# Kernel optimization log

Hardware: AMD Instinct MI355X
Metric: run time of the kernel (lower is better)

Reference implementation:

```python
import jax, jax.numpy as jnp
import numpy as np

D_MODEL = 1024
N_HEADS = 16
D_HEAD = D_MODEL // N_HEADS
B = 2
Q_LEN = 1024
MEM_LEN = 1024
K_LEN = MEM_LEN + Q_LEN


def _split_heads(x, n_heads):
    b, t, d = x.shape
    return x.reshape(b, t, n_heads, d // n_heads).transpose(0, 2, 1, 3)


def _rel_shift(x):
    # x: [b, h, q, k] -> Transformer-XL relative shift
    b, h, q_len, k_len = x.shape
    x = jnp.pad(x, ((0, 0), (0, 0), (0, 0), (1, 0)))
    x = x.reshape(b, h, k_len + 1, q_len)
    x = x[:, :, 1:, :]
    return x.reshape(b, h, q_len, k_len)


def setup_inputs() -> dict:
    key = jax.random.key(0)
    ks = jax.random.split(key, 10)
    s = 1.0 / np.sqrt(D_MODEL)  # lecun_normal-ish scale for kernels
    return {
        "h": jax.random.normal(ks[0], (B, Q_LEN, D_MODEL), jnp.float32),
        "mem": jax.random.normal(ks[1], (B, MEM_LEN, D_MODEL), jnp.float32),
        "r": jax.random.normal(ks[2], (K_LEN, D_MODEL), jnp.float32),
        "Wq": jax.random.normal(ks[3], (D_MODEL, D_MODEL), jnp.float32) * s,
        "Wk": jax.random.normal(ks[4], (D_MODEL, D_MODEL), jnp.float32) * s,
        "Wv": jax.random.normal(ks[5], (D_MODEL, D_MODEL), jnp.float32) * s,
        "Wr": jax.random.normal(ks[6], (D_MODEL, D_MODEL), jnp.float32) * s,
        "Wo": jax.random.normal(ks[7], (D_MODEL, D_MODEL), jnp.float32) * s,
        "r_w_bias": jnp.zeros((N_HEADS, D_HEAD), jnp.float32),
        "r_r_bias": jnp.zeros((N_HEADS, D_HEAD), jnp.float32),
    }


def reference(h, mem, r, Wq, Wk, Wv, Wr, Wo, r_w_bias, r_r_bias):
    k_len = mem.shape[1] + h.shape[1]
    cat = jnp.concatenate([mem, h], axis=1)           # [b, k, d]
    q = _split_heads(h @ Wq, N_HEADS)                  # [b, h, q, dh]
    k = _split_heads(cat @ Wk, N_HEADS)                # [b, h, k, dh]
    v = _split_heads(cat @ Wv, N_HEADS)                # [b, h, k, dh]
    r_head = (r @ Wr).reshape(k_len, N_HEADS, D_HEAD).transpose(1, 0, 2)  # [h, k, dh]

    qw = q + r_w_bias[None, :, None, :]
    ac = jnp.einsum('bhqd,bhkd->bhqk', qw, k)          # content score
    qr = q + r_r_bias[None, :, None, :]
    bd = _rel_shift(jnp.einsum('bhqd,hkd->bhqk', qr, r_head))  # position score

    attn_score = (ac + bd) / jnp.sqrt(jnp.array(D_HEAD, jnp.float32))
    attn_prob = jax.nn.softmax(attn_score, axis=-1)
    attn_vec = jnp.einsum('bhqk,bhkd->bhqd', attn_prob, v)
    b, nh, t, dh = attn_vec.shape
    attn_vec = attn_vec.transpose(0, 2, 1, 3).reshape(b, t, nh * dh)
    return attn_vec @ Wo
```

## Files before the change

kernel.cpp:

```cpp
#include <hip/hip_runtime.h>

#define DM 1024
#define NH 16
#define DH 64
#define QL 1024
#define KL 2048

typedef short s16x8 __attribute__((ext_vector_type(8)));
typedef float f32x4 __attribute__((ext_vector_type(4)));
typedef unsigned int u32x4 __attribute__((ext_vector_type(4)));

__device__ __forceinline__ unsigned short f2bf(float f) {
  unsigned int u = __builtin_bit_cast(unsigned int, f);
  u += 0x7fffu + ((u >> 16) & 1u);
  return (unsigned short)(u >> 16);
}
__device__ __forceinline__ float bf2f(unsigned short b) {
  unsigned int u = ((unsigned int)b) << 16;
  return __builtin_bit_cast(float, u);
}
__device__ __forceinline__ f32x4 mfma16(s16x8 a, s16x8 b, f32x4 c) {
  return __builtin_amdgcn_mfma_f32_16x16x32_bf16(a, b, c, 0, 0, 0);
}
__device__ __forceinline__ void gl2lds16(const void* g, void* l) {
  __builtin_amdgcn_global_load_lds(
      (const __attribute__((address_space(1))) unsigned int*)g,
      (__attribute__((address_space(3))) unsigned int*)l, 16, 0, 0);
}


__global__ __launch_bounds__(256) void prep_all(
    const float* __restrict__ h, const float* __restrict__ mem, const float* __restrict__ r,
    const float* __restrict__ Wq, const float* __restrict__ Wk, const float* __restrict__ Wv,
    const float* __restrict__ Wr, const float* __restrict__ Wo,
    unsigned short* __restrict__ catb, unsigned short* __restrict__ rb,
    unsigned short* __restrict__ wqt, unsigned short* __restrict__ wkvt,
    unsigned short* __restrict__ wrt,
    unsigned short* __restrict__ wohi, unsigned short* __restrict__ wolo)
{
  __shared__ unsigned short tH[64][72];
  __shared__ unsigned short tL[64][72];
  if (blockIdx.x < 6144) {
    int idx = blockIdx.x * 256 + threadIdx.x;
    if (idx < 1048576) {
      int e = idx * 4;
      int row = e >> 10, col = e & 1023;
      int b = row >> 11, t = row & 2047;
      const float* s = (t < 1024) ? &mem[((size_t)(b * 1024 + t)) * 1024 + col]
                                  : &h[((size_t)(b * 1024 + t - 1024)) * 1024 + col];
      float4 v = *(const float4*)s;
      *(ushort4*)&catb[e] = make_ushort4(f2bf(v.x), f2bf(v.y), f2bf(v.z), f2bf(v.w));
    } else {
      int e = (idx - 1048576) * 4;
      float4 v = *(const float4*)&r[e];
      *(ushort4*)&rb[e] = make_ushort4(f2bf(v.x), f2bf(v.y), f2bf(v.z), f2bf(v.w));
    }
    return;
  }
  int q = blockIdx.x - 6144;
  int job = q >> 8;
  int tb = q & 255;
  int sr0 = (tb >> 4) * 64, sc0 = (tb & 15) * 64;
  const float* src = (job == 0) ? Wq : (job == 1) ? Wk : (job == 2) ? Wv : (job == 3) ? Wr : Wo;
  int tid = threadIdx.x;
  int rr = tid >> 4, c4 = (tid & 15) * 4;
#pragma unroll
  for (int i = 0; i < 4; ++i) {
    int row = rr + i * 16;
    float4 v = *(const float4*)&src[(size_t)(sr0 + row) * 1024 + sc0 + c4];
    float vv[4] = {v.x, v.y, v.z, v.w};
#pragma unroll
    for (int j = 0; j < 4; ++j) {
      unsigned short hi = f2bf(vv[j]);
      tH[c4 + j][row] = hi;
      if (job == 4) tL[c4 + j][row] = f2bf(vv[j] - bf2f(hi));
    }
  }
  __syncthreads();
  unsigned short* dst = (job == 0) ? wqt : (job == 1) ? wkvt
                      : (job == 2) ? (wkvt + (size_t)1024 * 1024)
                      : (job == 3) ? wrt : wohi;
#pragma unroll
  for (int i = 0; i < 4; ++i) {
    int row = rr + i * 16;
    size_t o = (size_t)(sc0 + row) * 1024 + sr0 + c4;
    *(ushort4*)&dst[o] = make_ushort4(tH[row][c4], tH[row][c4 + 1], tH[row][c4 + 2], tH[row][c4 + 3]);
    if (job == 4)
      *(ushort4*)&wolo[o] = make_ushort4(tL[row][c4], tL[row][c4 + 1], tL[row][c4 + 2], tL[row][c4 + 3]);
  }
}

__global__ __launch_bounds__(256) void gemm_all(
    const unsigned short* __restrict__ catb, const unsigned short* __restrict__ rb,
    const unsigned short* __restrict__ wqt, const unsigned short* __restrict__ wkvt,
    const unsigned short* __restrict__ wrt,
    const float* __restrict__ rwb, const float* __restrict__ rrb,
    unsigned short* __restrict__ qwP, unsigned short* __restrict__ qrP,
    unsigned short* __restrict__ kP, unsigned short* __restrict__ vP,
    unsigned short* __restrict__ rP)
{
  __shared__ __align__(16) unsigned short As[2][128 * 32];
  __shared__ __align__(16) unsigned short Bs[2][128 * 32];
  int blk = blockIdx.x, tid = threadIdx.x;
  int job, mb, nb;
  const unsigned short *A, *Bt;
  if (blk < 128)      { job = 0; A = catb; Bt = wqt;  mb = blk >> 3; nb = blk & 7; }
  else if (blk < 640) { job = 1; A = catb; Bt = wkvt; int q = blk - 128; mb = q >> 4; nb = q & 15; }
  else                { job = 2; A = rb;   Bt = wrt;  int q = blk - 640; mb = q >> 3; nb = q & 7; }

  const int w = tid >> 6;
  const int r0 = tid >> 2;
  const int c0u = (tid & 3) * 8;
  int ga_r0 = mb * 128 + r0, ga_r1 = mb * 128 + 64 + r0;
  if (job == 0) {
    ga_r0 = ((ga_r0 >> 10) << 11) + 1024 + (ga_r0 & 1023);
    ga_r1 = ((ga_r1 >> 10) << 11) + 1024 + (ga_r1 & 1023);
  }
  const unsigned short* gA0 = A + (size_t)ga_r0 * 1024 + c0u;
  const unsigned short* gA1 = A + (size_t)ga_r1 * 1024 + c0u;
  const unsigned short* gB0 = Bt + (size_t)(nb * 128 + r0) * 1024 + c0u;
  const unsigned short* gB1 = Bt + (size_t)(nb * 128 + 64 + r0) * 1024 + c0u;

  const int lane = tid & 63;
  const int lc = lane & 15, quad = lane >> 4;
  const int wm = (w & 1) * 64, wn = (w >> 1) * 64;

  auto stage = [&](int k0, int bi) {
    gl2lds16(gA0 + k0, (char*)As[bi] + w * 1024);
    gl2lds16(gA1 + k0, (char*)As[bi] + 4096 + w * 1024);
    gl2lds16(gB0 + k0, (char*)Bs[bi] + w * 1024);
    gl2lds16(gB1 + k0, (char*)Bs[bi] + 4096 + w * 1024);
  };

  f32x4 acc[4][4];
#pragma unroll
  for (int mt = 0; mt < 4; ++mt)
#pragma unroll
    for (int nt = 0; nt < 4; ++nt) { acc[mt][nt][0] = 0.f; acc[mt][nt][1] = 0.f; acc[mt][nt][2] = 0.f; acc[mt][nt][3] = 0.f; }

  stage(0, 0);
  __syncthreads();
  for (int k0 = 0; k0 < 1024; k0 += 32) {
    int cur = (k0 >> 5) & 1;
    if (k0 + 32 < 1024) stage(k0 + 32, cur ^ 1);
    s16x8 af[4], bfr[4];
#pragma unroll
    for (int mt = 0; mt < 4; ++mt) af[mt] = *(const s16x8*)&As[cur][(wm + mt * 16 + lc) * 32 + quad * 8];
#pragma unroll
    for (int nt = 0; nt < 4; ++nt) bfr[nt] = *(const s16x8*)&Bs[cur][(wn + nt * 16 + lc) * 32 + quad * 8];
#pragma unroll
    for (int mt = 0; mt < 4; ++mt)
#pragma unroll
      for (int nt = 0; nt < 4; ++nt) acc[mt][nt] = mfma16(af[mt], bfr[nt], acc[mt][nt]);
    __syncthreads();
  }

#pragma unroll
  for (int mt = 0; mt < 4; ++mt) {
    int t4 = mb * 128 + wm + mt * 16 + quad * 4;
#pragma unroll
    for (int nt = 0; nt < 4; ++nt) {
      int n = nb * 128 + wn + nt * 16 + lc;
      if (job == 0) {
        int hh = n >> 6, dh = n & 63;
        int f = dh >> 5, qd = (dh >> 3) & 3, j = dh & 7;
        float bw = rwb[n], br = rrb[n];
        int bb = t4 >> 10, trow = t4 & 1023;
        size_t tbb = ((((size_t)(bb * NH + hh) * 64 + (trow >> 4)) * 2 + f) * 512) + qd * 128 + j;
        int l0 = trow & 15;
#pragma unroll
        for (int rr = 0; rr < 4; ++rr) {
          qwP[tbb + (l0 + rr) * 8] = f2bf(acc[mt][nt][rr] + bw);
          qrP[tbb + (l0 + rr) * 8] = f2bf(acc[mt][nt][rr] + br);
        }
      } else if (job == 1) {
        int bb = t4 >> 11, t = t4 & 2047;
        if (n < 1024) {
          int hh = n >> 6, dh = n & 63;
          int f = dh >> 5, qd = (dh >> 3) & 3, j = dh & 7;
          size_t tbb = ((((size_t)(bb * NH + hh) * 128 + (t >> 4)) * 2 + f) * 512) + qd * 128 + j;
          int l0 = t & 15;
#pragma unroll
          for (int rr = 0; rr < 4; ++rr)
            kP[tbb + (l0 + rr) * 8] = f2bf(acc[mt][nt][rr]);
        } else {
          int n2 = n - 1024, hh = n2 >> 6, dh = n2 & 63;
          int bhv = bb * NH + hh;
          int kt = t >> 5;
          int ntv = dh >> 4;
          int lanev = (((t >> 2) & 3) << 4) + (dh & 15);
          int elemv = ((t >> 4) & 1) << 2;
          ushort4 pk = make_ushort4(f2bf(acc[mt][nt][0]), f2bf(acc[mt][nt][1]),
                                    f2bf(acc[mt][nt][2]), f2bf(acc[mt][nt][3]));
          *(ushort4*)&vP[(((size_t)bhv * 64 + kt) * 4 + ntv) * 512 + lanev * 8 + elemv] = pk;
        }
      } else {
        int hh = n >> 6, dh = n & 63;
        int f = dh >> 5, qd = (dh >> 3) & 3, j = dh & 7;
        size_t tbb = (((size_t)hh * 128 + (t4 >> 4)) * 2 + f) * 512 + qd * 128 + j;
        int l0 = t4 & 15;
#pragma unroll
        for (int rr = 0; rr < 4; ++rr)
          rP[tbb + (l0 + rr) * 8] = f2bf(acc[mt][nt][rr]);
      }
    }
  }
}

#define BDSTR 2060
#define OSTR 65
__global__ __launch_bounds__(512, 4) void attn(
    const unsigned short* __restrict__ qwP, const unsigned short* __restrict__ qrP,
    const unsigned short* __restrict__ kP, const unsigned short* __restrict__ vP,
    const unsigned short* __restrict__ rP,
    unsigned short* __restrict__ avhi, unsigned short* __restrict__ avlo)
{
  __shared__ __align__(16) unsigned short bdS[16 * BDSTR];
  float* oS = (float*)bdS;
  float* lS = (float*)bdS + 8 * 16 * OSTR;

  const int tid = threadIdx.x;
  const int w = tid >> 6, lane = tid & 63;
  const int lc = lane & 15, quad = lane >> 4;
  const int sem = (blockIdx.x & 7) * 256 + (blockIdx.x >> 3);
  const int is = sem & 63, h = (sem >> 6) & 15, b = sem >> 10;
  const int i0 = is * 16;
  const size_t bh = (size_t)b * NH + h;

  const unsigned short* qwP_p = qwP + bh * 65536;
  const unsigned short* qrP_p = qrP + bh * 65536;
  const unsigned short* kP_p  = kP + bh * 131072;
  const unsigned short* vP_p  = vP + bh * (size_t)KL * DH + lane * 8;
  const unsigned short* rP_p  = rP + (size_t)h * 131072;

  if (tid < 16) {
    int kz = i0 + tid + 1025;
    if (kz < 2048) bdS[tid * BDSTR + kz] = 0;
  }

  {
    const int cmax = 1006 - i0;
    s16x8 qa00 = *(const s16x8*)(qrP_p + is * 1024 + lane * 8);
    s16x8 qa01 = *(const s16x8*)(qrP_p + is * 1024 + 512 + lane * 8);
    int r1 = i0 + 16 + lc; if (r1 > 1023) r1 = 1023;
    int off1 = (r1 >> 4) * 1024 + (quad * 16 + (r1 & 15)) * 8;
    s16x8 qa10 = *(const s16x8*)(qrP_p + off1);
    s16x8 qa11 = *(const s16x8*)(qrP_p + off1 + 512);
    const int xt0 = w * 16;
    const unsigned short* rp = rP_p + xt0 * 1024 + lane * 8;
    s16x8 rf0 = *(const s16x8*)rp;
    s16x8 rf1 = *(const s16x8*)(rp + 512);
    const int rbq = quad * 4 * BDSTR;
    for (int xt = xt0; xt < xt0 + 16; ++xt) {
      s16x8 cf0 = rf0, cf1 = rf1;
      if (xt + 1 < xt0 + 16) {
        const unsigned short* rpn = rP_p + (xt + 1) * 1024 + lane * 8;
        rf0 = *(const s16x8*)rpn;
        rf1 = *(const s16x8*)(rpn + 512);
      }
      f32x4 c0; c0[0] = 0.f; c0[1] = 0.f; c0[2] = 0.f; c0[3] = 0.f;
      c0 = mfma16(qa00, cf0, c0); c0 = mfma16(qa01, cf1, c0);
      int c = xt * 16 + lc;
#pragma unroll
      for (int rr = 0; rr < 4; ++rr) {
        int row = quad * 4 + rr;
        int s = c + i0 + row - 1023;
        int off = (s < 0) ? (s - 12) : s;
        if (!(row == 0 && s < 0))
          bdS[rbq + rr * BDSTR + off] = f2bf(c0[rr]);
      }
      if (xt * 16 <= cmax) {
        f32x4 c1; c1[0] = 0.f; c1[1] = 0.f; c1[2] = 0.f; c1[3] = 0.f;
        c1 = mfma16(qa10, cf0, c1); c1 = mfma16(qa11, cf1, c1);
        if (lane < 16) {
          int key2 = c + i0 + 1041;
          if (key2 < 2048) bdS[15 * BDSTR + key2] = f2bf(c1[0]);
        }
      }
    }
  }
  __syncthreads();

  s16x8 qwf0 = *(const s16x8*)(qwP_p + is * 1024 + lane * 8);
  s16x8 qwf1 = *(const s16x8*)(qwP_p + is * 1024 + 512 + lane * 8);

  f32x4 O[4];
#pragma unroll
  for (int nt = 0; nt < 4; ++nt) { O[nt][0] = 0.f; O[nt][1] = 0.f; O[nt][2] = 0.f; O[nt][3] = 0.f; }
  float lsumQ = 0.f;

  const unsigned short* bdlane = bdS + lc * BDSTR + quad * 4;
  const int base = w * 256;
  const float E2S = 0.18033688011112042f;
  const float E2B = -17.312340490667562f;

  auto loadK4 = [&](int k0, s16x8& a0, s16x8& a1, s16x8& b0, s16x8& b1) {
    const unsigned short* kp = kP_p + (size_t)(k0 >> 4) * 1024 + lane * 8;
    a0 = *(const s16x8*)kp;
    a1 = *(const s16x8*)(kp + 512);
    b0 = *(const s16x8*)(kp + 1024);
    b1 = *(const s16x8*)(kp + 1536);
  };
  auto loadV4 = [&](int k0, s16x8& x0, s16x8& x1, s16x8& x2, s16x8& x3) {
    const unsigned short* bp = vP_p + (size_t)(k0 >> 5) * 2048;
    x0 = *(const s16x8*)bp;
    x1 = *(const s16x8*)(bp + 512);
    x2 = *(const s16x8*)(bp + 1024);
    x3 = *(const s16x8*)(bp + 1536);
  };

  s16x8 ka0, ka1, kb0, kb1, v0, v1, v2, v3;
  uint2 bq0 = *(const uint2*)(bdlane + base);
  uint2 bq1 = *(const uint2*)(bdlane + base + 16);
  loadK4(base, ka0, ka1, kb0, kb1);
  loadV4(base, v0, v1, v2, v3);

#pragma unroll 1
  for (int s = 0; s < 8; ++s) {
    const int k0 = base + s * 32;
    const int kn = (s < 7) ? (k0 + 32) : k0;
    uint2 nq0 = *(const uint2*)(bdlane + kn);
    uint2 nq1 = *(const uint2*)(bdlane + kn + 16);
    s16x8 na0, na1, nb0, nb1;  loadK4(kn, na0, na1, nb0, nb1);
    s16x8 nv0, nv1, nv2, nv3;  loadV4(kn, nv0, nv1, nv2, nv3);

    __builtin_amdgcn_s_setprio(1);
    f32x4 c;
    c[0] = __builtin_bit_cast(float, bq0.x << 16);
    c[1] = __builtin_bit_cast(float, bq0.x & 0xFFFF0000u);
    c[2] = __builtin_bit_cast(float, bq0.y << 16);
    c[3] = __builtin_bit_cast(float, bq0.y & 0xFFFF0000u);
    c = mfma16(ka0, qwf0, c);
    c = mfma16(ka1, qwf1, c);
    f32x4 d;
    d[0] = __builtin_bit_cast(float, bq1.x << 16);
    d[1] = __builtin_bit_cast(float, bq1.x & 0xFFFF0000u);
    d[2] = __builtin_bit_cast(float, bq1.y << 16);
    d[3] = __builtin_bit_cast(float, bq1.y & 0xFFFF0000u);
    d = mfma16(kb0, qwf0, d);
    d = mfma16(kb1, qwf1, d);
    __builtin_amdgcn_s_setprio(0);

    float p0[4], p1[4];
#pragma unroll
    for (int rr = 0; rr < 4; ++rr) {
      p0[rr] = __builtin_amdgcn_exp2f(fmaf(c[rr], E2S, E2B));
      p1[rr] = __builtin_amdgcn_exp2f(fmaf(d[rr], E2S, E2B));
    }
    lsumQ += ((p0[0] + p0[1]) + (p0[2] + p0[3])) + ((p1[0] + p1[1]) + (p1[2] + p1[3]));

    unsigned int w0, w1, w2, w3;
    asm("v_cvt_pk_bf16_f32 %0, %1, %2" : "=v"(w0) : "v"(p0[0]), "v"(p0[1]));
    asm("v_cvt_pk_bf16_f32 %0, %1, %2" : "=v"(w1) : "v"(p0[2]), "v"(p0[3]));
    asm("v_cvt_pk_bf16_f32 %0, %1, %2" : "=v"(w2) : "v"(p1[0]), "v"(p1[1]));
    asm("v_cvt_pk_bf16_f32 %0, %1, %2" : "=v"(w3) : "v"(p1[2]), "v"(p1[3]));
    u32x4 pw4 = {w0, w1, w2, w3};
    s16x8 pf = __builtin_bit_cast(s16x8, pw4);

    __builtin_amdgcn_s_setprio(1);
    O[0] = mfma16(v0, pf, O[0]);
    O[1] = mfma16(v1, pf, O[1]);
    O[2] = mfma16(v2, pf, O[2]);
    O[3] = mfma16(v3, pf, O[3]);
    __builtin_amdgcn_s_setprio(0);

    bq0 = nq0; bq1 = nq1;
    ka0 = na0; ka1 = na1; kb0 = nb0; kb1 = nb1;
    v0 = nv0; v1 = nv1; v2 = nv2; v3 = nv3;
  }

  lsumQ += __shfl_xor(lsumQ, 16);
  lsumQ += __shfl_xor(lsumQ, 32);

  __syncthreads();
#pragma unroll
  for (int nt = 0; nt < 4; ++nt)
#pragma unroll
    for (int rr = 0; rr < 4; ++rr)
      oS[(w * 16 + lc) * OSTR + nt * 16 + quad * 4 + rr] = O[nt][rr];
  if (lane < 16) lS[w * 16 + lc] = lsumQ;
  __syncthreads();

  if (tid < 256) {
    int r = tid >> 4, c0 = (tid & 15) * 4;
    float L = 0.f, a0 = 0.f, a1 = 0.f, a2 = 0.f, a3 = 0.f;
#pragma unroll
    for (int wv = 0; wv < 8; ++wv) {
      L += lS[wv * 16 + r];
      const float* op = oS + (wv * 16 + r) * OSTR + c0;
      a0 += op[0]; a1 += op[1]; a2 += op[2]; a3 += op[3];
    }
    float inv = 1.0f / L;
    float v[4] = {a0 * inv, a1 * inv, a2 * inv, a3 * inv};
    unsigned short hi[4], lo[4];
#pragma unroll
    for (int j = 0; j < 4; ++j) {
      hi[j] = f2bf(v[j]);
      lo[j] = f2bf(v[j] - bf2f(hi[j]));
    }
    size_t oidx = ((size_t)(b * QL + i0 + r)) * DM + h * DH + c0;
    *(ushort4*)&avhi[oidx] = make_ushort4(hi[0], hi[1], hi[2], hi[3]);
    *(ushort4*)&avlo[oidx] = make_ushort4(lo[0], lo[1], lo[2], lo[3]);
  }
}

__global__ __launch_bounds__(256) void gemm_final(
    const unsigned short* __restrict__ avhi, const unsigned short* __restrict__ avlo,
    const unsigned short* __restrict__ wohi, const unsigned short* __restrict__ wolo,
    float* __restrict__ out)
{
  __shared__ __align__(16) unsigned short S[2][4][64 * 32];
  int tid = threadIdx.x;
  int sem = (blockIdx.x & 7) * 64 + (blockIdx.x >> 3);
  int mb = sem >> 4, nb = sem & 15;

  const int w = tid >> 6, lane = tid & 63;
  const int srow = w * 16 + (lane >> 2);
  const int scu = (lane & 3) * 8;
  const size_t arow = (size_t)(mb * 64 + srow) * 1024 + scu;
  const size_t brow = (size_t)(nb * 64 + srow) * 1024 + scu;

  const int lc = lane & 15, quad = lane >> 4;
  const int wm = (w & 1) * 32, wn = (w >> 1) * 32;

  auto stage = [&](int k0, int bi) {
    gl2lds16(avhi + arow + k0, (char*)S[bi][0] + w * 1024);
    gl2lds16(avlo + arow + k0, (char*)S[bi][1] + w * 1024);
    gl2lds16(wohi + brow + k0, (char*)S[bi][2] + w * 1024);
    gl2lds16(wolo + brow + k0, (char*)S[bi][3] + w * 1024);
  };

  f32x4 acc[2][2];
#pragma unroll
  for (int mt = 0; mt < 2; ++mt)
#pragma unroll
    for (int nt = 0; nt < 2; ++nt) { acc[mt][nt][0] = 0.f; acc[mt][nt][1] = 0.f; acc[mt][nt][2] = 0.f; acc[mt][nt][3] = 0.f; }

  stage(0, 0);
  __syncthreads();
  for (int k0 = 0; k0 < 1024; k0 += 32) {
    int cur = (k0 >> 5) & 1;
    if (k0 + 32 < 1024) stage(k0 + 32, cur ^ 1);
    s16x8 ah[2], al[2], bh[2], bl[2];
#pragma unroll
    for (int mt = 0; mt < 2; ++mt) {
      int off = (wm + mt * 16 + lc) * 32 + quad * 8;
      ah[mt] = *(const s16x8*)&S[cur][0][off];
      al[mt] = *(const s16x8*)&S[cur][1][off];
    }
#pragma unroll
    for (int nt = 0; nt < 2; ++nt) {
      int off = (wn + nt * 16 + lc) * 32 + quad * 8;
      bh[nt] = *(const s16x8*)&S[cur][2][off];
      bl[nt] = *(const s16x8*)&S[cur][3][off];
    }
#pragma unroll
    for (int mt = 0; mt < 2; ++mt)
#pragma unroll
      for (int nt = 0; nt < 2; ++nt) {
        acc[mt][nt] = mfma16(ah[mt], bh[nt], acc[mt][nt]);
        acc[mt][nt] = mfma16(ah[mt], bl[nt], acc[mt][nt]);
        acc[mt][nt] = mfma16(al[mt], bh[nt], acc[mt][nt]);
      }
    __syncthreads();
  }

#pragma unroll
  for (int mt = 0; mt < 2; ++mt)
#pragma unroll
    for (int nt = 0; nt < 2; ++nt) {
      int n = nb * 64 + wn + nt * 16 + lc;
#pragma unroll
      for (int rr = 0; rr < 4; ++rr) {
        int m = mb * 64 + wm + mt * 16 + quad * 4 + rr;
        out[(size_t)m * 1024 + n] = acc[mt][nt][rr];
      }
    }
}

extern "C" void kernel_launch(void* const* d_in, const int* in_sizes, int n_in,
                              void* d_out, int out_size, void* d_ws, size_t ws_size,
                              hipStream_t stream) {
  (void)in_sizes; (void)n_in; (void)out_size; (void)ws_size;
  const float* h   = (const float*)d_in[0];
  const float* mem = (const float*)d_in[1];
  const float* r   = (const float*)d_in[2];
  const float* Wq  = (const float*)d_in[3];
  const float* Wk  = (const float*)d_in[4];
  const float* Wv  = (const float*)d_in[5];
  const float* Wr  = (const float*)d_in[6];
  const float* Wo  = (const float*)d_in[7];
  const float* rwb = (const float*)d_in[8];
  const float* rrb = (const float*)d_in[9];
  float* out = (float*)d_out;

  char* ws = (char*)d_ws;
  unsigned short* catb = (unsigned short*)(ws + 0);
  unsigned short* rb   = (unsigned short*)(ws + 8388608);
  unsigned short* wqt  = (unsigned short*)(ws + 12582912);
  unsigned short* wkvt = (unsigned short*)(ws + 14680064);
  unsigned short* wrt  = (unsigned short*)(ws + 18874368);
  unsigned short* wohi = (unsigned short*)(ws + 20971520);
  unsigned short* wolo = (unsigned short*)(ws + 23068672);
  unsigned short* qwP  = (unsigned short*)(ws + 25165824);
  unsigned short* qrP  = (unsigned short*)(ws + 29360128);
  unsigned short* kPb  = (unsigned short*)(ws + 33554432);
  unsigned short* vPb  = (unsigned short*)(ws + 41943040);
  unsigned short* rPb  = (unsigned short*)(ws + 50331648);
  unsigned short* avhi = (unsigned short*)(ws + 54525952);
  unsigned short* avlo = (unsigned short*)(ws + 58720256);

  prep_all<<<7424, 256, 0, stream>>>(h, mem, r, Wq, Wk, Wv, Wr, Wo,
                                     catb, rb, wqt, wkvt, wrt, wohi, wolo);
  gemm_all<<<768, 256, 0, stream>>>(catb, rb, wqt, wkvt, wrt, rwb, rrb,
                                    qwP, qrP, kPb, vPb, rPb);
  attn<<<2048, 512, 0, stream>>>(qwP, qrP, kPb, vPb, rPb, avhi, avlo);
  gemm_final<<<512, 256, 0, stream>>>(avhi, avlo, wohi, wolo, out);
}
```

Before: 229.2 us.

## Split bd score buffer into two key halves to halve LDS and raise occupancy

The attention kernel now builds the relative-position score buffer in shared memory for one half of the key range at a time. It computes that half's positional scores and then runs the QK/softmax/PV loop over it. This halves the LDS footprint (row stride 2060 to 1060), so launch bounds go from 4 to 6 blocks per CU for more occupancy. The cost is an extra barrier pair per half, more complex index mapping for the shifted positions, and rP fetches that are no longer software-prefetched. The setprio hints around the MFMAs were also removed.

```diff
diff --git a/kernel.cpp b/kernel.cpp
--- a/kernel.cpp
+++ b/kernel.cpp
@@ -207,9 +207,9 @@
   }
 }
 
-#define BDSTR 2060
+#define BDSTR 1060
 #define OSTR 65
-__global__ __launch_bounds__(512, 4) void attn(
+__global__ __launch_bounds__(512, 6) void attn(
     const unsigned short* __restrict__ qwP, const unsigned short* __restrict__ qrP,
     const unsigned short* __restrict__ kP, const unsigned short* __restrict__ vP,
     const unsigned short* __restrict__ rP,
@@ -233,54 +233,6 @@
   const unsigned short* vP_p  = vP + bh * (size_t)KL * DH + lane * 8;
   const unsigned short* rP_p  = rP + (size_t)h * 131072;
 
-  if (tid < 16) {
-    int kz = i0 + tid + 1025;
-    if (kz < 2048) bdS[tid * BDSTR + kz] = 0;
-  }
-
-  {
-    const int cmax = 1006 - i0;
-    s16x8 qa00 = *(const s16x8*)(qrP_p + is * 1024 + lane * 8);
-    s16x8 qa01 = *(const s16x8*)(qrP_p + is * 1024 + 512 + lane * 8);
-    int r1 = i0 + 16 + lc; if (r1 > 1023) r1 = 1023;
-    int off1 = (r1 >> 4) * 1024 + (quad * 16 + (r1 & 15)) * 8;
-    s16x8 qa10 = *(const s16x8*)(qrP_p + off1);
-    s16x8 qa11 = *(const s16x8*)(qrP_p + off1 + 512);
-    const int xt0 = w * 16;
-    const unsigned short* rp = rP_p + xt0 * 1024 + lane * 8;
-    s16x8 rf0 = *(const s16x8*)rp;
-    s16x8 rf1 = *(const s16x8*)(rp + 512);
-    const int rbq = quad * 4 * BDSTR;
-    for (int xt = xt0; xt < xt0 + 16; ++xt) {
-      s16x8 cf0 = rf0, cf1 = rf1;
-      if (xt + 1 < xt0 + 16) {
-        const unsigned short* rpn = rP_p + (xt + 1) * 1024 + lane * 8;
-        rf0 = *(const s16x8*)rpn;
-        rf1 = *(const s16x8*)(rpn + 512);
-      }
-      f32x4 c0; c0[0] = 0.f; c0[1] = 0.f; c0[2] = 0.f; c0[3] = 0.f;
-      c0 = mfma16(qa00, cf0, c0); c0 = mfma16(qa01, cf1, c0);
-      int c = xt * 16 + lc;
-#pragma unroll
-      for (int rr = 0; rr < 4; ++rr) {
-        int row = quad * 4 + rr;
-        int s = c + i0 + row - 1023;
-        int off = (s < 0) ? (s - 12) : s;
-        if (!(row == 0 && s < 0))
-          bdS[rbq + rr * BDSTR + off] = f2bf(c0[rr]);
-      }
-      if (xt * 16 <= cmax) {
-        f32x4 c1; c1[0] = 0.f; c1[1] = 0.f; c1[2] = 0.f; c1[3] = 0.f;
-        c1 = mfma16(qa10, cf0, c1); c1 = mfma16(qa11, cf1, c1);
-        if (lane < 16) {
-          int key2 = c + i0 + 1041;
-          if (key2 < 2048) bdS[15 * BDSTR + key2] = f2bf(c1[0]);
-        }
-      }
-    }
-  }
-  __syncthreads();
-
   s16x8 qwf0 = *(const s16x8*)(qwP_p + is * 1024 + lane * 8);
   s16x8 qwf1 = *(const s16x8*)(qwP_p + is * 1024 + 512 + lane * 8);
 
@@ -290,7 +242,8 @@
   float lsumQ = 0.f;
 
   const unsigned short* bdlane = bdS + lc * BDSTR + quad * 4;
-  const int base = w * 256;
+  const int rbq = quad * 4 * BDSTR;
+  const int cmax = 1006 - i0;
   const float E2S = 0.18033688011112042f;
   const float E2B = -17.312340490667562f;
 
@@ -309,64 +262,130 @@
     x3 = *(const s16x8*)(bp + 1536);
   };
 
-  s16x8 ka0, ka1, kb0, kb1, v0, v1, v2, v3;
-  uint2 bq0 = *(const uint2*)(bdlane + base);
-  uint2 bq1 = *(const uint2*)(bdlane + base + 16);
-  loadK4(base, ka0, ka1, kb0, kb1);
-  loadV4(base, v0, v1, v2, v3);
-
 #pragma unroll 1
-  for (int s = 0; s < 8; ++s) {
-    const int k0 = base + s * 32;
-    const int kn = (s < 7) ? (k0 + 32) : k0;
-    uint2 nq0 = *(const uint2*)(bdlane + kn);
-    uint2 nq1 = *(const uint2*)(bdlane + kn + 16);
-    s16x8 na0, na1, nb0, nb1;  loadK4(kn, na0, na1, nb0, nb1);
-    s16x8 nv0, nv1, nv2, nv3;  loadV4(kn, nv0, nv1, nv2, nv3);
-
-    __builtin_amdgcn_s_setprio(1);
-    f32x4 c;
-    c[0] = __builtin_bit_cast(float, bq0.x << 16);
-    c[1] = __builtin_bit_cast(float, bq0.x & 0xFFFF0000u);
-    c[2] = __builtin_bit_cast(float, bq0.y << 16);
-    c[3] = __builtin_bit_cast(float, bq0.y & 0xFFFF0000u);
-    c = mfma16(ka0, qwf0, c);
-    c = mfma16(ka1, qwf1, c);
-    f32x4 d;
-    d[0] = __builtin_bit_cast(float, bq1.x << 16);
-    d[1] = __builtin_bit_cast(float, bq1.x & 0xFFFF0000u);
-    d[2] = __builtin_bit_cast(float, bq1.y << 16);
-    d[3] = __builtin_bit_cast(float, bq1.y & 0xFFFF0000u);
-    d = mfma16(kb0, qwf0, d);
-    d = mfma16(kb1, qwf1, d);
-    __builtin_amdgcn_s_setprio(0);
-
-    float p0[4], p1[4];
-#pragma unroll
-    for (int rr = 0; rr < 4; ++rr) {
-      p0[rr] = __builtin_amdgcn_exp2f(fmaf(c[rr], E2S, E2B));
-      p1[rr] = __builtin_amdgcn_exp2f(fmaf(d[rr], E2S, E2B));
-    }
-    lsumQ += ((p0[0] + p0[1]) + (p0[2] + p0[3])) + ((p1[0] + p1[1]) + (p1[2] + p1[3]));
-
-    unsigned int w0, w1, w2, w3;
-    asm("v_cvt_pk_bf16_f32 %0, %1, %2" : "=v"(w0) : "v"(p0[0]), "v"(p0[1]));
-    asm("v_cvt_pk_bf16_f32 %0, %1, %2" : "=v"(w1) : "v"(p0[2]), "v"(p0[3]));
-    asm("v_cvt_pk_bf16_f32 %0, %1, %2" : "=v"(w2) : "v"(p1[0]), "v"(p1[1]));
-    asm("v_cvt_pk_bf16_f32 %0, %1, %2" : "=v"(w3) : "v"(p1[2]), "v"(p1[3]));
-    u32x4 pw4 = {w0, w1, w2, w3};
-    s16x8 pf = __builtin_bit_cast(s16x8, pw4);
-
-    __builtin_amdgcn_s_setprio(1);
-    O[0] = mfma16(v0, pf, O[0]);
-    O[1] = mfma16(v1, pf, O[1]);
-    O[2] = mfma16(v2, pf, O[2]);
-    O[3] = mfma16(v3, pf, O[3]);
-    __builtin_amdgcn_s_setprio(0);
-
-    bq0 = nq0; bq1 = nq1;
-    ka0 = na0; ka1 = na1; kb0 = nb0; kb1 = nb1;
-    v0 = nv0; v1 = nv1; v2 = nv2; v3 = nv3;
+  for (int H = 0; H < 2; ++H) {
+    if (H) __syncthreads();
+
+    if (H && tid < 16) {
+      int kz = i0 + tid + 1025;
+      if (kz < 2048) bdS[tid * BDSTR + (kz - 1024)] = 0;
+    }
+    {
+      s16x8 qa00 = *(const s16x8*)(qrP_p + is * 1024 + lane * 8);
+      s16x8 qa01 = *(const s16x8*)(qrP_p + is * 1024 + 512 + lane * 8);
+      int n, xA_hi = 0, xB_lo = 0, xbase = 0;
+      if (H == 0) {
+        xbase = (1008 - i0) >> 4;
+        n = ((2046 - i0) >> 4) - xbase + 1;
+      } else {
+        xA_hi = (1022 - i0) >> 4;
+        xB_lo = (2032 - i0) >> 4;
+        n = (xA_hi + 1) + (128 - xB_lo);
+      }
+      s16x8 qa10, qa11;
+      if (H) {
+        int r1 = i0 + 16 + lc; if (r1 > 1023) r1 = 1023;
+        int off1 = (r1 >> 4) * 1024 + (quad * 16 + (r1 & 15)) * 8;
+        qa10 = *(const s16x8*)(qrP_p + off1);
+        qa11 = *(const s16x8*)(qrP_p + off1 + 512);
+      }
+#pragma unroll 1
+      for (int j = 0; j < 9; ++j) {
+        int t = w + 8 * j;
+        if (t >= n) break;
+        int xt = (H == 0) ? (xbase + t)
+                          : ((t <= xA_hi) ? t : (xB_lo + (t - xA_hi - 1)));
+        const unsigned short* rp = rP_p + xt * 1024 + lane * 8;
+        s16x8 cf0 = *(const s16x8*)rp;
+        s16x8 cf1 = *(const s16x8*)(rp + 512);
+        f32x4 c0; c0[0] = 0.f; c0[1] = 0.f; c0[2] = 0.f; c0[3] = 0.f;
+        c0 = mfma16(qa00, cf0, c0); c0 = mfma16(qa01, cf1, c0);
+        int c = xt * 16 + lc;
+        if (H == 0) {
+#pragma unroll
+          for (int rr = 0; rr < 4; ++rr) {
+            int row = quad * 4 + rr;
+            int s = c + i0 + row - 1023;
+            if ((unsigned)s < 1024u)
+              bdS[rbq + rr * BDSTR + s] = f2bf(c0[rr]);
+          }
+        } else {
+#pragma unroll
+          for (int rr = 0; rr < 4; ++rr) {
+            int s = c + i0 + quad * 4 + rr - 1023;
+            int off = (s >= 1024) ? (s - 1024) : (s - 36);
+            if (s >= 1024 || (s < 0 && (quad | rr) != 0))
+              bdS[rbq + rr * BDSTR + off] = f2bf(c0[rr]);
+          }
+          if (xt * 16 <= cmax) {
+            f32x4 c1; c1[0] = 0.f; c1[1] = 0.f; c1[2] = 0.f; c1[3] = 0.f;
+            c1 = mfma16(qa10, cf0, c1); c1 = mfma16(qa11, cf1, c1);
+            if (lane < 16) {
+              int key2 = c + i0 + 1041;
+              if (key2 < 2048) bdS[15 * BDSTR + (key2 - 1024)] = f2bf(c1[0]);
+            }
+          }
+        }
+      }
+    }
+    __syncthreads();
+
+    const int kg0 = H * 1024 + w * 128;
+    const int kc0 = w * 128;
+    s16x8 ka0, ka1, kb0, kb1, v0, v1, v2, v3;
+    uint2 bq0 = *(const uint2*)(bdlane + kc0);
+    uint2 bq1 = *(const uint2*)(bdlane + kc0 + 16);
+    loadK4(kg0, ka0, ka1, kb0, kb1);
+    loadV4(kg0, v0, v1, v2, v3);
+
+#pragma unroll 1
+    for (int s = 0; s < 4; ++s) {
+      const int dn = (s < 3) ? (s + 1) * 32 : s * 32;
+      uint2 nq0 = *(const uint2*)(bdlane + kc0 + dn);
+      uint2 nq1 = *(const uint2*)(bdlane + kc0 + dn + 16);
+      s16x8 na0, na1, nb0, nb1;  loadK4(kg0 + dn, na0, na1, nb0, nb1);
+      s16x8 nv0, nv1, nv2, nv3;  loadV4(kg0 + dn, nv0, nv1, nv2, nv3);
+
+      f32x4 c;
+      c[0] = __builtin_bit_cast(float, bq0.x << 16);
+      c[1] = __builtin_bit_cast(float, bq0.x & 0xFFFF0000u);
+      c[2] = __builtin_bit_cast(float, bq0.y << 16);
+      c[3] = __builtin_bit_cast(float, bq0.y & 0xFFFF0000u);
+      c = mfma16(ka0, qwf0, c);
+      c = mfma16(ka1, qwf1, c);
+      f32x4 d;
+      d[0] = __builtin_bit_cast(float, bq1.x << 16);
+      d[1] = __builtin_bit_cast(float, bq1.x & 0xFFFF0000u);
+      d[2] = __builtin_bit_cast(float, bq1.y << 16);
+      d[3] = __builtin_bit_cast(float, bq1.y & 0xFFFF0000u);
+      d = mfma16(kb0, qwf0, d);
+      d = mfma16(kb1, qwf1, d);
+
+      float p0[4], p1[4];
+#pragma unroll
+      for (int rr = 0; rr < 4; ++rr) {
+        p0[rr] = __builtin_amdgcn_exp2f(fmaf(c[rr], E2S, E2B));
+        p1[rr] = __builtin_amdgcn_exp2f(fmaf(d[rr], E2S, E2B));
+      }
+      lsumQ += ((p0[0] + p0[1]) + (p0[2] + p0[3])) + ((p1[0] + p1[1]) + (p1[2] + p1[3]));
+
+      unsigned int w0, w1, w2, w3;
+      asm("v_cvt_pk_bf16_f32 %0, %1, %2" : "=v"(w0) : "v"(p0[0]), "v"(p0[1]));
+      asm("v_cvt_pk_bf16_f32 %0, %1, %2" : "=v"(w1) : "v"(p0[2]), "v"(p0[3]));
+      asm("v_cvt_pk_bf16_f32 %0, %1, %2" : "=v"(w2) : "v"(p1[0]), "v"(p1[1]));
+      asm("v_cvt_pk_bf16_f32 %0, %1, %2" : "=v"(w3) : "v"(p1[2]), "v"(p1[3]));
+      u32x4 pw4 = {w0, w1, w2, w3};
+      s16x8 pf = __builtin_bit_cast(s16x8, pw4);
+
+      O[0] = mfma16(v0, pf, O[0]);
+      O[1] = mfma16(v1, pf, O[1]);
+      O[2] = mfma16(v2, pf, O[2]);
+      O[3] = mfma16(v3, pf, O[3]);
+
+      bq0 = nq0; bq1 = nq1;
+      ka0 = na0; ka1 = na1; kb0 = nb0; kb1 = nb1;
+      v0 = nv0; v1 = nv1; v2 = nv2; v3 = nv3;
+    }
   }
 
   lsumQ += __shfl_xor(lsumQ, 16);
```

After: 246.2 us. 1.07x slower.
